# Kernel optimization log

Measured on AMD Instinct MI355X. Metric: run time of the kernel, lower is better.

The kernel has to match this reference:

```python
import jax, jax.numpy as jnp
import numpy as np

B, T, D, U = 2048, 200, 128, 128  # batch, history len, input dim, gru units


def setup_inputs() -> dict:
    key = jax.random.key(0)
    ks = jax.random.split(key, 5)
    s = 1.0 / np.sqrt(U + D)
    return {
        "history_state": jax.random.normal(ks[0], (B, T, D), jnp.float32),
        "attention_score": jax.random.uniform(ks[1], (B, T, 1), jnp.float32),
        "Wu": jax.random.normal(ks[2], (U + D, U), jnp.float32) * s,
        "bu": jnp.zeros((U,), jnp.float32),
        "Wr": jax.random.normal(ks[3], (U + D, U), jnp.float32) * s,
        "br": jnp.zeros((U,), jnp.float32),
        "Wh": jax.random.normal(ks[4], (D + U, U), jnp.float32) * s,
        "bh": jnp.zeros((U,), jnp.float32),
    }


def reference(history_state, attention_score, Wu, bu, Wr, br, Wh, bh):
    # time-major for scan: (T, B, ...)
    xs = jnp.swapaxes(history_state, 0, 1)       # (T, B, D)
    ats = jnp.swapaxes(attention_score, 0, 1)    # (T, B, 1)
    h0 = jnp.zeros((history_state.shape[0], Wu.shape[1]), history_state.dtype)

    def step(h, xa):
        x, a = xa
        hx = jnp.concatenate([h, x], axis=-1)                       # (B, U+D)
        u = jax.nn.sigmoid(hx @ Wu + bu)                            # update gate
        r = jax.nn.sigmoid(hx @ Wr + br)                            # reset gate
        hh = jnp.tanh(jnp.concatenate([x, r * h], axis=-1) @ Wh + bh)
        u = u * a                                                   # attention-modulated update
        h_new = u * hh + (1.0 - u) * h
        return h_new, None

    h_final, _ = jax.lax.scan(step, h0, (xs, ats))
    return h_final  # (B, U)
```

## Files before the change

### kernel.cpp

```cpp
#include <hip/hip_runtime.h>
#include <hip/hip_bf16.h>


#define T_LEN 200
#define D_DIM 128
#define U_DIM 128
#define BM    16
#define CH    12
#define KCS   136
#define XSTEP (16 * KCS)

typedef __attribute__((ext_vector_type(8))) short bf16x8;
typedef __attribute__((ext_vector_type(4))) float f32x4;
typedef __attribute__((ext_vector_type(4))) unsigned int uint4v;

static __device__ __forceinline__ unsigned short f2bf(float f) {
    unsigned int u = __builtin_bit_cast(unsigned int, f);
    u += 0x7fffu + ((u >> 16) & 1u);
    return (unsigned short)(u >> 16);
}
static __device__ __forceinline__ unsigned int pkbf2(float a, float b) {
    float2 t; t.x = a; t.y = b;
    __hip_bfloat162 v = __float22bfloat162_rn(t);
    unsigned int u; __builtin_memcpy(&u, &v, 4);
    return u;
}
static __device__ __forceinline__ uint4v pack8u(float4 lo, float4 hi) {
    uint4v v;
    v[0] = pkbf2(lo.x, lo.y); v[1] = pkbf2(lo.z, lo.w);
    v[2] = pkbf2(hi.x, hi.y); v[3] = pkbf2(hi.z, hi.w);
    return v;
}
static __device__ __forceinline__ float fast_exp2(float x) {
#if __has_builtin(__builtin_amdgcn_exp2f)
    return __builtin_amdgcn_exp2f(x);
#else
    return exp2f(x);
#endif
}
static __device__ __forceinline__ float fast_rcp(float x) {
#if __has_builtin(__builtin_amdgcn_rcpf)
    return __builtin_amdgcn_rcpf(x);
#else
    return 1.0f / x;
#endif
}

__global__ __launch_bounds__(512, 2)
void gru_scan_kernel(const float* __restrict__ X,
                     const float* __restrict__ Att,
                     const float* __restrict__ Wu, const float* __restrict__ bu,
                     const float* __restrict__ Wr, const float* __restrict__ br,
                     const float* __restrict__ Wh, const float* __restrict__ bh,
                     float* __restrict__ out)
{
    __shared__ __align__(16) unsigned short x_sm[CH * XSTEP];
    __shared__ __align__(16) unsigned short h_bf[XSTEP];
    __shared__ __align__(16) unsigned short rh_bf[XSTEP];
    __shared__ float a_sm[CH * BM];

    const int tid  = threadIdx.x;
    const int wave = tid >> 6;
    const int lane = tid & 63;
    const int q    = lane >> 4;
    const int ln   = lane & 15;
    const int b0   = blockIdx.x * BM;

    const float INVLN2 = 1.4426950408889634f;

    bf16x8 wu[8], wr[8], wh[8];
    f32x4 nbu, nbr, bh2;
    {
        const int tb = 16 * wave;
        const int c  = tb + ln;
        const f32x4 bu4 = *(const f32x4*)&bu[tb + 4 * q];
        const f32x4 br4 = *(const f32x4*)&br[tb + 4 * q];
        const f32x4 bh4 = *(const f32x4*)&bh[tb + 4 * q];
        #pragma unroll
        for (int r = 0; r < 4; ++r) {
            nbu[r] = -bu4[r] * INVLN2;
            nbr[r] = -br4[r] * INVLN2;
            bh2[r] = 2.0f * bh4[r] * INVLN2;
        }
        #pragma unroll
        for (int kt = 0; kt < 8; ++kt) {
            const int k0 = 32 * kt + 8 * q;
            bf16x8 vu, vr, vh;
            #pragma unroll
            for (int j = 0; j < 8; ++j) {
                vu[j] = (short)f2bf(Wu[(k0 + j) * U_DIM + c] * -INVLN2);
                vr[j] = (short)f2bf(Wr[(k0 + j) * U_DIM + c] * -INVLN2);
                vh[j] = (short)f2bf(Wh[(k0 + j) * U_DIM + c] * (2.0f * INVLN2));
            }
            wu[kt] = vu; wr[kt] = vr; wh[kt] = vh;
        }
    }

    float hreg[4] = {0.f, 0.f, 0.f, 0.f};

    {
        unsigned int* hz = (unsigned int*)h_bf;
        unsigned int* rz = (unsigned int*)rh_bf;
        for (int i = tid; i < XSTEP / 2; i += 512) { hz[i] = 0; rz[i] = 0; }
    }

    const int s2   = tid >> 8;
    const int srow = (tid >> 4) & 15;
    const int cs   = tid & 15;
    const float* xbase = X + (size_t)(b0 + srow) * T_LEN * D_DIM + cs * 8;

    int t0 = 0;
    for (int ch = 0; ch < (T_LEN + CH - 1) / CH; ++ch) {
        const int L = (t0 + CH <= T_LEN) ? CH : (T_LEN - t0);

        {
            float4 px[12];
            #pragma unroll
            for (int w2 = 0; w2 < CH / 2; ++w2) {
                int t = t0 + 2 * w2 + s2;
                t = (t < T_LEN) ? t : (T_LEN - 1);
                const float* src = xbase + (size_t)t * D_DIM;
                px[2 * w2]     = *(const float4*)(src);
                px[2 * w2 + 1] = *(const float4*)(src + 4);
            }
            float a_px = 0.0f;
            if (tid < BM * CH) {
                int t = t0 + (tid >> 4);
                t = (t < T_LEN) ? t : (T_LEN - 1);
                a_px = Att[(size_t)(b0 + (tid & 15)) * T_LEN + t];
            }
            #pragma unroll
            for (int w2 = 0; w2 < CH / 2; ++w2) {
                const int s = 2 * w2 + s2;
                *(uint4v*)&x_sm[s * XSTEP + cs * KCS + srow * 8] =
                    pack8u(px[2 * w2], px[2 * w2 + 1]);
            }
            if (tid < BM * CH) a_sm[tid] = a_px;
        }
        __syncthreads();

        f32x4 acc_r, acc_u, acc_h;
        {
            bf16x8 xf[4];
            #pragma unroll
            for (int kt = 0; kt < 4; ++kt)
                xf[kt] = *(const bf16x8*)&x_sm[(4 * kt + q) * KCS + ln * 8];
            acc_r = nbr; acc_u = nbu; acc_h = bh2;
            #pragma unroll
            for (int kt = 0; kt < 4; ++kt) {
                acc_r = __builtin_amdgcn_mfma_f32_16x16x32_bf16(wr[kt + 4], xf[kt], acc_r, 0, 0, 0);
                acc_u = __builtin_amdgcn_mfma_f32_16x16x32_bf16(wu[kt + 4], xf[kt], acc_u, 0, 0, 0);
                acc_h = __builtin_amdgcn_mfma_f32_16x16x32_bf16(wh[kt],     xf[kt], acc_h, 0, 0, 0);
            }
        }

        for (int s = 0; s < L; ++s) {
            bf16x8 hf[4];
            #pragma unroll
            for (int kt = 0; kt < 4; ++kt)
                hf[kt] = *(const bf16x8*)&h_bf[(4 * kt + q) * KCS + ln * 8];
            const float a_att = a_sm[s * BM + ln];

            f32x4 ra = acc_r, rb = (f32x4)0.0f;
            ra = __builtin_amdgcn_mfma_f32_16x16x32_bf16(wr[0], hf[0], ra, 0, 0, 0);
            rb = __builtin_amdgcn_mfma_f32_16x16x32_bf16(wr[2], hf[2], rb, 0, 0, 0);
            ra = __builtin_amdgcn_mfma_f32_16x16x32_bf16(wr[1], hf[1], ra, 0, 0, 0);
            rb = __builtin_amdgcn_mfma_f32_16x16x32_bf16(wr[3], hf[3], rb, 0, 0, 0);
            #pragma unroll
            for (int kt = 0; kt < 4; ++kt)
                acc_u = __builtin_amdgcn_mfma_f32_16x16x32_bf16(wu[kt], hf[kt], acc_u, 0, 0, 0);

            {
                float rh[4];
                #pragma unroll
                for (int r = 0; r < 4; ++r) {
                    float zr = ra[r] + rb[r];
                    float rv = fast_rcp(1.0f + fast_exp2(zr));
                    rh[r] = rv * hreg[r];
                }
                uint2 wv; wv.x = pkbf2(rh[0], rh[1]); wv.y = pkbf2(rh[2], rh[3]);
                const int c8 = 2 * wave + (q >> 1);
                *(uint2*)&rh_bf[c8 * KCS + ln * 8 + (q & 1) * 4] = wv;
            }
            __syncthreads();

            bf16x8 rf[4];
            #pragma unroll
            for (int kt = 0; kt < 4; ++kt)
                rf[kt] = *(const bf16x8*)&rh_bf[(4 * kt + q) * KCS + ln * 8];

            float uq[4];
            #pragma unroll
            for (int r = 0; r < 4; ++r) {
                float u = fast_rcp(1.0f + fast_exp2(acc_u[r]));
                uq[r] = u * a_att;
            }

            f32x4 ha = acc_h, hb = (f32x4)0.0f;
            ha = __builtin_amdgcn_mfma_f32_16x16x32_bf16(wh[4], rf[0], ha, 0, 0, 0);
            hb = __builtin_amdgcn_mfma_f32_16x16x32_bf16(wh[6], rf[2], hb, 0, 0, 0);
            ha = __builtin_amdgcn_mfma_f32_16x16x32_bf16(wh[5], rf[1], ha, 0, 0, 0);
            hb = __builtin_amdgcn_mfma_f32_16x16x32_bf16(wh[7], rf[3], hb, 0, 0, 0);

            #pragma unroll
            for (int r = 0; r < 4; ++r) {
                float z  = ha[r] + hb[r];
                float hh = 1.0f - 2.0f * fast_rcp(1.0f + fast_exp2(z));
                float ho = hreg[r];
                hreg[r] = ho + uq[r] * (hh - ho);
            }
            {
                uint2 wv; wv.x = pkbf2(hreg[0], hreg[1]); wv.y = pkbf2(hreg[2], hreg[3]);
                const int c8 = 2 * wave + (q >> 1);
                *(uint2*)&h_bf[c8 * KCS + ln * 8 + (q & 1) * 4] = wv;
            }

            if (s + 1 < L) {
                bf16x8 xf[4];
                #pragma unroll
                for (int kt = 0; kt < 4; ++kt)
                    xf[kt] = *(const bf16x8*)&x_sm[(s + 1) * XSTEP + (4 * kt + q) * KCS + ln * 8];
                acc_r = nbr; acc_u = nbu; acc_h = bh2;
                #pragma unroll
                for (int kt = 0; kt < 4; ++kt) {
                    acc_r = __builtin_amdgcn_mfma_f32_16x16x32_bf16(wr[kt + 4], xf[kt], acc_r, 0, 0, 0);
                    acc_u = __builtin_amdgcn_mfma_f32_16x16x32_bf16(wu[kt + 4], xf[kt], acc_u, 0, 0, 0);
                    acc_h = __builtin_amdgcn_mfma_f32_16x16x32_bf16(wh[kt],     xf[kt], acc_h, 0, 0, 0);
                }
            }
            __syncthreads();
        }
        t0 += CH;
    }

    {
        f32x4 v;
        #pragma unroll
        for (int r = 0; r < 4; ++r) v[r] = hreg[r];
        *(f32x4*)&out[(size_t)(b0 + ln) * U_DIM + 16 * wave + 4 * q] = v;
    }
}

extern "C" void kernel_launch(void* const* d_in, const int* in_sizes, int n_in,
                              void* d_out, int out_size, void* d_ws, size_t ws_size,
                              hipStream_t stream) {
    const float* X   = (const float*)d_in[0];
    const float* Att = (const float*)d_in[1];
    const float* Wu  = (const float*)d_in[2];
    const float* bu  = (const float*)d_in[3];
    const float* Wr  = (const float*)d_in[4];
    const float* br  = (const float*)d_in[5];
    const float* Wh  = (const float*)d_in[6];
    const float* bh  = (const float*)d_in[7];
    float* out = (float*)d_out;

    gru_scan_kernel<<<dim3(2048 / BM), dim3(512), 0, stream>>>(
        X, Att, Wu, bu, Wr, br, Wh, bh, out);
}
```

Baseline: 459.3 us.

## Halve waves per block, stream x directly into registers with prefetch, peel first step

The block shrinks from 8 to 4 waves, so each wave owns two 16-column output tiles and holds twice the weight fragments in registers. The chunked LDS staging of x and attention is removed: each lane loads its own x row for the next timestep straight from global memory into registers, and attention is read through a small rolling prefetch queue. The x-projection MFMAs are recomputed every step inside the loop, and __syncthreads is replaced by a raw LDS waitcnt plus s_barrier. The first timestep is peeled using h0=0, which drops the LDS zeroing and the reset-gate work at t=0. The exchange is more register pressure and less occupancy (launch bounds 256,1) in return for fewer barriers and no LDS traffic for x; global load latency now has to hide behind a single step of compute.

```diff
diff --git a/kernel.cpp b/kernel.cpp
--- a/kernel.cpp
+++ b/kernel.cpp
@@ -6,13 +6,14 @@
 #define D_DIM 128
 #define U_DIM 128
 #define BM    16
-#define CH    12
 #define KCS   136
 #define XSTEP (16 * KCS)
 
 typedef __attribute__((ext_vector_type(8))) short bf16x8;
 typedef __attribute__((ext_vector_type(4))) float f32x4;
 typedef __attribute__((ext_vector_type(4))) unsigned int uint4v;
+
+#define MFMA __builtin_amdgcn_mfma_f32_16x16x32_bf16
 
 static __device__ __forceinline__ unsigned short f2bf(float f) {
     unsigned int u = __builtin_bit_cast(unsigned int, f);
@@ -25,11 +26,11 @@
     unsigned int u; __builtin_memcpy(&u, &v, 4);
     return u;
 }
-static __device__ __forceinline__ uint4v pack8u(float4 lo, float4 hi) {
+static __device__ __forceinline__ bf16x8 pack8bf(f32x4 lo, f32x4 hi) {
     uint4v v;
-    v[0] = pkbf2(lo.x, lo.y); v[1] = pkbf2(lo.z, lo.w);
-    v[2] = pkbf2(hi.x, hi.y); v[3] = pkbf2(hi.z, hi.w);
-    return v;
+    v[0] = pkbf2(lo[0], lo[1]); v[1] = pkbf2(lo[2], lo[3]);
+    v[2] = pkbf2(hi[0], hi[1]); v[3] = pkbf2(hi[2], hi[3]);
+    return __builtin_bit_cast(bf16x8, v);
 }
 static __device__ __forceinline__ float fast_exp2(float x) {
 #if __has_builtin(__builtin_amdgcn_exp2f)
@@ -45,8 +46,14 @@
     return 1.0f / x;
 #endif
 }
-
-__global__ __launch_bounds__(512, 2)
+static __device__ __forceinline__ void block_sync_lds() {
+    asm volatile("s_waitcnt lgkmcnt(0)" ::: "memory");
+    __builtin_amdgcn_sched_barrier(0);
+    __builtin_amdgcn_s_barrier();
+    __builtin_amdgcn_sched_barrier(0);
+}
+
+__global__ __launch_bounds__(256, 1)
 void gru_scan_kernel(const float* __restrict__ X,
                      const float* __restrict__ Att,
                      const float* __restrict__ Wu, const float* __restrict__ bu,
@@ -54,10 +61,8 @@
                      const float* __restrict__ Wh, const float* __restrict__ bh,
                      float* __restrict__ out)
 {
-    __shared__ __align__(16) unsigned short x_sm[CH * XSTEP];
     __shared__ __align__(16) unsigned short h_bf[XSTEP];
     __shared__ __align__(16) unsigned short rh_bf[XSTEP];
-    __shared__ float a_sm[CH * BM];
 
     const int tid  = threadIdx.x;
     const int wave = tid >> 6;
@@ -68,19 +73,20 @@
 
     const float INVLN2 = 1.4426950408889634f;
 
-    bf16x8 wu[8], wr[8], wh[8];
-    f32x4 nbu, nbr, bh2;
-    {
-        const int tb = 16 * wave;
+    bf16x8 wu[2][8], wr[2][8], wh[2][8];
+    f32x4 nbu[2], nbr[2], bh2[2];
+    #pragma unroll
+    for (int tl = 0; tl < 2; ++tl) {
+        const int tb = 32 * wave + 16 * tl;
         const int c  = tb + ln;
         const f32x4 bu4 = *(const f32x4*)&bu[tb + 4 * q];
         const f32x4 br4 = *(const f32x4*)&br[tb + 4 * q];
         const f32x4 bh4 = *(const f32x4*)&bh[tb + 4 * q];
         #pragma unroll
         for (int r = 0; r < 4; ++r) {
-            nbu[r] = -bu4[r] * INVLN2;
-            nbr[r] = -br4[r] * INVLN2;
-            bh2[r] = 2.0f * bh4[r] * INVLN2;
+            nbu[tl][r] = -bu4[r] * INVLN2;
+            nbr[tl][r] = -br4[r] * INVLN2;
+            bh2[tl][r] = 2.0f * bh4[r] * INVLN2;
         }
         #pragma unroll
         for (int kt = 0; kt < 8; ++kt) {
@@ -92,152 +98,154 @@
                 vr[j] = (short)f2bf(Wr[(k0 + j) * U_DIM + c] * -INVLN2);
                 vh[j] = (short)f2bf(Wh[(k0 + j) * U_DIM + c] * (2.0f * INVLN2));
             }
-            wu[kt] = vu; wr[kt] = vr; wh[kt] = vh;
-        }
-    }
-
-    float hreg[4] = {0.f, 0.f, 0.f, 0.f};
+            wu[tl][kt] = vu; wr[tl][kt] = vr; wh[tl][kt] = vh;
+        }
+    }
+
+    const float* xrow = X + (size_t)(b0 + ln) * T_LEN * D_DIM + 8 * q;
+    const float* arow = Att + (size_t)(b0 + ln) * T_LEN;
+
+    f32x4 px[8];
+    #pragma unroll
+    for (int kt = 0; kt < 4; ++kt) {
+        px[2 * kt]     = *(const f32x4*)(xrow + 32 * kt);
+        px[2 * kt + 1] = *(const f32x4*)(xrow + 32 * kt + 4);
+    }
+    const float a0 = arow[0];
+    float attA = arow[1], attB = arow[2], attC = arow[3];
+
+    float hreg[2][4];
+
+    const int c8base = (4 * wave) * KCS + ln * 8 + (q & 1) * 4;
+    const int c8q    = (q >> 1) * KCS;
 
     {
-        unsigned int* hz = (unsigned int*)h_bf;
-        unsigned int* rz = (unsigned int*)rh_bf;
-        for (int i = tid; i < XSTEP / 2; i += 512) { hz[i] = 0; rz[i] = 0; }
-    }
-
-    const int s2   = tid >> 8;
-    const int srow = (tid >> 4) & 15;
-    const int cs   = tid & 15;
-    const float* xbase = X + (size_t)(b0 + srow) * T_LEN * D_DIM + cs * 8;
-
-    int t0 = 0;
-    for (int ch = 0; ch < (T_LEN + CH - 1) / CH; ++ch) {
-        const int L = (t0 + CH <= T_LEN) ? CH : (T_LEN - t0);
-
+        bf16x8 xf[4];
+        #pragma unroll
+        for (int kt = 0; kt < 4; ++kt) xf[kt] = pack8bf(px[2 * kt], px[2 * kt + 1]);
+        #pragma unroll
+        for (int kt = 0; kt < 4; ++kt) {
+            px[2 * kt]     = *(const f32x4*)(xrow + D_DIM + 32 * kt);
+            px[2 * kt + 1] = *(const f32x4*)(xrow + D_DIM + 32 * kt + 4);
+        }
+        #pragma unroll
+        for (int tl = 0; tl < 2; ++tl) {
+            f32x4 xu = nbu[tl], xh = bh2[tl];
+            #pragma unroll
+            for (int kt = 0; kt < 4; ++kt) {
+                xu = MFMA(wu[tl][kt + 4], xf[kt], xu, 0, 0, 0);
+                xh = MFMA(wh[tl][kt],     xf[kt], xh, 0, 0, 0);
+            }
+            #pragma unroll
+            for (int r = 0; r < 4; ++r) {
+                float u  = fast_rcp(1.0f + fast_exp2(xu[r])) * a0;
+                float hh = 1.0f - 2.0f * fast_rcp(1.0f + fast_exp2(xh[r]));
+                hreg[tl][r] = u * hh;
+            }
+            uint2 wv; wv.x = pkbf2(hreg[tl][0], hreg[tl][1]);
+            wv.y = pkbf2(hreg[tl][2], hreg[tl][3]);
+            *(uint2*)&h_bf[c8base + c8q + 2 * tl * KCS] = wv;
+        }
+    }
+    block_sync_lds();
+
+    for (int t = 1; t < T_LEN; ++t) {
+        bf16x8 hf[4];
+        #pragma unroll
+        for (int kt = 0; kt < 4; ++kt)
+            hf[kt] = *(const bf16x8*)&h_bf[(4 * kt + q) * KCS + ln * 8];
+
+        bf16x8 xf[4];
+        #pragma unroll
+        for (int kt = 0; kt < 4; ++kt) xf[kt] = pack8bf(px[2 * kt], px[2 * kt + 1]);
         {
-            float4 px[12];
-            #pragma unroll
-            for (int w2 = 0; w2 < CH / 2; ++w2) {
-                int t = t0 + 2 * w2 + s2;
-                t = (t < T_LEN) ? t : (T_LEN - 1);
-                const float* src = xbase + (size_t)t * D_DIM;
-                px[2 * w2]     = *(const float4*)(src);
-                px[2 * w2 + 1] = *(const float4*)(src + 4);
-            }
-            float a_px = 0.0f;
-            if (tid < BM * CH) {
-                int t = t0 + (tid >> 4);
-                t = (t < T_LEN) ? t : (T_LEN - 1);
-                a_px = Att[(size_t)(b0 + (tid & 15)) * T_LEN + t];
-            }
-            #pragma unroll
-            for (int w2 = 0; w2 < CH / 2; ++w2) {
-                const int s = 2 * w2 + s2;
-                *(uint4v*)&x_sm[s * XSTEP + cs * KCS + srow * 8] =
-                    pack8u(px[2 * w2], px[2 * w2 + 1]);
-            }
-            if (tid < BM * CH) a_sm[tid] = a_px;
-        }
-        __syncthreads();
-
-        f32x4 acc_r, acc_u, acc_h;
-        {
-            bf16x8 xf[4];
+            const int tn = (t + 1 < T_LEN) ? t + 1 : T_LEN - 1;
+            const float* xs = xrow + (size_t)tn * D_DIM;
+            #pragma unroll
+            for (int kt = 0; kt < 4; ++kt) {
+                px[2 * kt]     = *(const f32x4*)(xs + 32 * kt);
+                px[2 * kt + 1] = *(const f32x4*)(xs + 32 * kt + 4);
+            }
+        }
+        const float a_att = attA;
+        attA = attB; attB = attC;
+        attC = arow[(t + 3 < T_LEN) ? t + 3 : T_LEN - 1];
+
+        f32x4 xr[2], xu[2], xh[2];
+        #pragma unroll
+        for (int tl = 0; tl < 2; ++tl) {
+            xr[tl] = nbr[tl]; xu[tl] = nbu[tl]; xh[tl] = bh2[tl];
+            #pragma unroll
+            for (int kt = 0; kt < 4; ++kt) {
+                xr[tl] = MFMA(wr[tl][kt + 4], xf[kt], xr[tl], 0, 0, 0);
+                xu[tl] = MFMA(wu[tl][kt + 4], xf[kt], xu[tl], 0, 0, 0);
+                xh[tl] = MFMA(wh[tl][kt],     xf[kt], xh[tl], 0, 0, 0);
+            }
+        }
+        f32x4 ra[2], rb[2];
+        #pragma unroll
+        for (int tl = 0; tl < 2; ++tl) {
+            ra[tl] = MFMA(wr[tl][0], hf[0], (f32x4)0.0f, 0, 0, 0);
+            rb[tl] = MFMA(wr[tl][2], hf[2], (f32x4)0.0f, 0, 0, 0);
+            ra[tl] = MFMA(wr[tl][1], hf[1], ra[tl], 0, 0, 0);
+            rb[tl] = MFMA(wr[tl][3], hf[3], rb[tl], 0, 0, 0);
             #pragma unroll
             for (int kt = 0; kt < 4; ++kt)
-                xf[kt] = *(const bf16x8*)&x_sm[(4 * kt + q) * KCS + ln * 8];
-            acc_r = nbr; acc_u = nbu; acc_h = bh2;
-            #pragma unroll
-            for (int kt = 0; kt < 4; ++kt) {
-                acc_r = __builtin_amdgcn_mfma_f32_16x16x32_bf16(wr[kt + 4], xf[kt], acc_r, 0, 0, 0);
-                acc_u = __builtin_amdgcn_mfma_f32_16x16x32_bf16(wu[kt + 4], xf[kt], acc_u, 0, 0, 0);
-                acc_h = __builtin_amdgcn_mfma_f32_16x16x32_bf16(wh[kt],     xf[kt], acc_h, 0, 0, 0);
-            }
-        }
-
-        for (int s = 0; s < L; ++s) {
-            bf16x8 hf[4];
-            #pragma unroll
-            for (int kt = 0; kt < 4; ++kt)
-                hf[kt] = *(const bf16x8*)&h_bf[(4 * kt + q) * KCS + ln * 8];
-            const float a_att = a_sm[s * BM + ln];
-
-            f32x4 ra = acc_r, rb = (f32x4)0.0f;
-            ra = __builtin_amdgcn_mfma_f32_16x16x32_bf16(wr[0], hf[0], ra, 0, 0, 0);
-            rb = __builtin_amdgcn_mfma_f32_16x16x32_bf16(wr[2], hf[2], rb, 0, 0, 0);
-            ra = __builtin_amdgcn_mfma_f32_16x16x32_bf16(wr[1], hf[1], ra, 0, 0, 0);
-            rb = __builtin_amdgcn_mfma_f32_16x16x32_bf16(wr[3], hf[3], rb, 0, 0, 0);
-            #pragma unroll
-            for (int kt = 0; kt < 4; ++kt)
-                acc_u = __builtin_amdgcn_mfma_f32_16x16x32_bf16(wu[kt], hf[kt], acc_u, 0, 0, 0);
-
-            {
-                float rh[4];
-                #pragma unroll
-                for (int r = 0; r < 4; ++r) {
-                    float zr = ra[r] + rb[r];
-                    float rv = fast_rcp(1.0f + fast_exp2(zr));
-                    rh[r] = rv * hreg[r];
-                }
-                uint2 wv; wv.x = pkbf2(rh[0], rh[1]); wv.y = pkbf2(rh[2], rh[3]);
-                const int c8 = 2 * wave + (q >> 1);
-                *(uint2*)&rh_bf[c8 * KCS + ln * 8 + (q & 1) * 4] = wv;
-            }
-            __syncthreads();
-
-            bf16x8 rf[4];
-            #pragma unroll
-            for (int kt = 0; kt < 4; ++kt)
-                rf[kt] = *(const bf16x8*)&rh_bf[(4 * kt + q) * KCS + ln * 8];
-
-            float uq[4];
+                xu[tl] = MFMA(wu[tl][kt], hf[kt], xu[tl], 0, 0, 0);
+        }
+        #pragma unroll
+        for (int tl = 0; tl < 2; ++tl) {
+            float rh[4];
             #pragma unroll
             for (int r = 0; r < 4; ++r) {
-                float u = fast_rcp(1.0f + fast_exp2(acc_u[r]));
-                uq[r] = u * a_att;
-            }
-
-            f32x4 ha = acc_h, hb = (f32x4)0.0f;
-            ha = __builtin_amdgcn_mfma_f32_16x16x32_bf16(wh[4], rf[0], ha, 0, 0, 0);
-            hb = __builtin_amdgcn_mfma_f32_16x16x32_bf16(wh[6], rf[2], hb, 0, 0, 0);
-            ha = __builtin_amdgcn_mfma_f32_16x16x32_bf16(wh[5], rf[1], ha, 0, 0, 0);
-            hb = __builtin_amdgcn_mfma_f32_16x16x32_bf16(wh[7], rf[3], hb, 0, 0, 0);
-
+                float zr = xr[tl][r] + ra[tl][r] + rb[tl][r];
+                float rv = fast_rcp(1.0f + fast_exp2(zr));
+                rh[r] = rv * hreg[tl][r];
+            }
+            uint2 wv; wv.x = pkbf2(rh[0], rh[1]); wv.y = pkbf2(rh[2], rh[3]);
+            *(uint2*)&rh_bf[c8base + c8q + 2 * tl * KCS] = wv;
+        }
+        block_sync_lds();
+
+        bf16x8 rf[4];
+        #pragma unroll
+        for (int kt = 0; kt < 4; ++kt)
+            rf[kt] = *(const bf16x8*)&rh_bf[(4 * kt + q) * KCS + ln * 8];
+
+        float uq[2][4];
+        #pragma unroll
+        for (int tl = 0; tl < 2; ++tl)
+            #pragma unroll
+            for (int r = 0; r < 4; ++r)
+                uq[tl][r] = fast_rcp(1.0f + fast_exp2(xu[tl][r])) * a_att;
+
+        #pragma unroll
+        for (int tl = 0; tl < 2; ++tl) {
+            f32x4 ha = xh[tl], hb = (f32x4)0.0f;
+            ha = MFMA(wh[tl][4], rf[0], ha, 0, 0, 0);
+            hb = MFMA(wh[tl][6], rf[2], hb, 0, 0, 0);
+            ha = MFMA(wh[tl][5], rf[1], ha, 0, 0, 0);
+            hb = MFMA(wh[tl][7], rf[3], hb, 0, 0, 0);
             #pragma unroll
             for (int r = 0; r < 4; ++r) {
                 float z  = ha[r] + hb[r];
                 float hh = 1.0f - 2.0f * fast_rcp(1.0f + fast_exp2(z));
-                float ho = hreg[r];
-                hreg[r] = ho + uq[r] * (hh - ho);
-            }
-            {
-                uint2 wv; wv.x = pkbf2(hreg[0], hreg[1]); wv.y = pkbf2(hreg[2], hreg[3]);
-                const int c8 = 2 * wave + (q >> 1);
-                *(uint2*)&h_bf[c8 * KCS + ln * 8 + (q & 1) * 4] = wv;
-            }
-
-            if (s + 1 < L) {
-                bf16x8 xf[4];
-                #pragma unroll
-                for (int kt = 0; kt < 4; ++kt)
-                    xf[kt] = *(const bf16x8*)&x_sm[(s + 1) * XSTEP + (4 * kt + q) * KCS + ln * 8];
-                acc_r = nbr; acc_u = nbu; acc_h = bh2;
-                #pragma unroll
-                for (int kt = 0; kt < 4; ++kt) {
-                    acc_r = __builtin_amdgcn_mfma_f32_16x16x32_bf16(wr[kt + 4], xf[kt], acc_r, 0, 0, 0);
-                    acc_u = __builtin_amdgcn_mfma_f32_16x16x32_bf16(wu[kt + 4], xf[kt], acc_u, 0, 0, 0);
-                    acc_h = __builtin_amdgcn_mfma_f32_16x16x32_bf16(wh[kt],     xf[kt], acc_h, 0, 0, 0);
-                }
-            }
-            __syncthreads();
-        }
-        t0 += CH;
-    }
-
-    {
+                float ho = hreg[tl][r];
+                hreg[tl][r] = ho + uq[tl][r] * (hh - ho);
+            }
+            uint2 wv; wv.x = pkbf2(hreg[tl][0], hreg[tl][1]);
+            wv.y = pkbf2(hreg[tl][2], hreg[tl][3]);
+            *(uint2*)&h_bf[c8base + c8q + 2 * tl * KCS] = wv;
+        }
+        block_sync_lds();
+    }
+
+    #pragma unroll
+    for (int tl = 0; tl < 2; ++tl) {
         f32x4 v;
         #pragma unroll
-        for (int r = 0; r < 4; ++r) v[r] = hreg[r];
-        *(f32x4*)&out[(size_t)(b0 + ln) * U_DIM + 16 * wave + 4 * q] = v;
+        for (int r = 0; r < 4; ++r) v[r] = hreg[tl][r];
+        *(f32x4*)&out[(size_t)(b0 + ln) * U_DIM + 32 * wave + 16 * tl + 4 * q] = v;
     }
 }
 
@@ -254,6 +262,6 @@
     const float* bh  = (const float*)d_in[7];
     float* out = (float*)d_out;
 
-    gru_scan_kernel<<<dim3(2048 / BM), dim3(512), 0, stream>>>(
+    gru_scan_kernel<<<dim3(2048 / BM), dim3(256), 0, stream>>>(
         X, Att, Wu, bu, Wr, br, Wh, bh, out);
 }
```

Measured after the change: 538.1 us. 17.2% more time.
